# Kernel optimization log

Hardware: AMD Instinct MI355X
Metric: run time of the kernel (lower is better)

Reference implementation:

```python
import jax, jax.numpy as jnp
import numpy as np

N_HEAD = 8
HEAD_DIM = 32  # 256 / 8
MASK_VALUE = -10000.0

def setup_inputs() -> dict:
    key = jax.random.key(0)
    k1, k2, k3 = jax.random.split(key, 3)
    B, S, D = 8, 2048, 256
    x = jax.random.normal(k1, (B, S, D), dtype=jnp.float32)
    # kaiming_normal fan_in-based std ~ sqrt(2/fan_in)
    w_qkv = jax.random.normal(k2, (3 * D, D), dtype=jnp.float32) * np.sqrt(2.0 / D)
    b_qkv = jnp.zeros((3 * D,), dtype=jnp.float32)
    w_out = jax.random.normal(k3, (D, D), dtype=jnp.float32) * np.sqrt(2.0 / D)
    b_out = jnp.zeros((D,), dtype=jnp.float32)
    return {"x": x, "w_qkv": w_qkv, "b_qkv": b_qkv, "w_out": w_out, "b_out": b_out}

def reference(x, w_qkv, b_qkv, w_out, b_out):
    B, S, D = x.shape
    qkv = x @ w_qkv.T + b_qkv                      # [B,S,3D]
    q, k, v = jnp.split(qkv, 3, axis=-1)           # each [B,S,D]
    def split_heads(t):
        return t.reshape(B, S, N_HEAD, HEAD_DIM).transpose(0, 2, 1, 3)  # [B,H,S,hd]
    q, k, v = split_heads(q), split_heads(k), split_heads(v)
    scores = jnp.einsum('bhqd,bhkd->bhqk', q, k) / jnp.sqrt(jnp.float32(HEAD_DIM))
    causal = jnp.tril(jnp.ones((S, S), dtype=bool))
    scores = jnp.where(causal[None, None], scores, jnp.float32(MASK_VALUE))
    attn = jax.nn.softmax(scores, axis=-1)          # dropout p=0 (eval)
    out = jnp.einsum('bhqk,bhkd->bhqd', attn, v)    # [B,H,S,hd]
    out = out.transpose(0, 2, 1, 3).reshape(B, S, D)  # merge heads
    out = out @ w_out.T + b_out
    return (out, attn)
```

## Files before the change

kernel.cpp:

```cpp
#include <hip/hip_runtime.h>
#include <cmath>

#define NB 8
#define NS 2048
#define ND 256
#define NH 8
#define HD 32
#define NM (NB*NS)
#define QS_LOG2 (0.17677669529663689f * 1.4426950408889634f)
#define OUT_ATTN ((size_t)NM * ND)

typedef __attribute__((ext_vector_type(8))) short bf16x8;
typedef __attribute__((ext_vector_type(4))) float f32x4;

__device__ __forceinline__ ushort f2b(float f) {
  union { float f; uint32_t u; } v; v.f = f;
  const uint32_t r = (v.u + 0x7FFFu + ((v.u >> 16) & 1u)) >> 16;
  return (ushort)r;
}
__device__ __forceinline__ float b2f(ushort u) {
  union { uint32_t u; float f; } v; v.u = ((uint32_t)u) << 16;
  return v.f;
}

__global__ __launch_bounds__(256) void prep_kernel(
    const float* __restrict__ x, const float* __restrict__ wq,
    const float* __restrict__ wo,
    ushort* __restrict__ xh, ushort* __restrict__ xl,
    ushort* __restrict__ wqh, ushort* __restrict__ wql,
    ushort* __restrict__ woh) {
  const int g = blockIdx.x * 256 + threadIdx.x;
  if (g < 1048576) {
    const float4 v = ((const float4*)x)[g];
    ushort4 h, l;
    h.x = f2b(v.x); l.x = f2b(v.x - b2f(h.x));
    h.y = f2b(v.y); l.y = f2b(v.y - b2f(h.y));
    h.z = f2b(v.z); l.z = f2b(v.z - b2f(h.z));
    h.w = f2b(v.w); l.w = f2b(v.w - b2f(h.w));
    ((ushort4*)xh)[g] = h; ((ushort4*)xl)[g] = l;
  } else if (g < 1048576 + 49152) {
    const int t = g - 1048576;
    const float4 v = ((const float4*)wq)[t];
    ushort4 h, l;
    h.x = f2b(v.x); l.x = f2b(v.x - b2f(h.x));
    h.y = f2b(v.y); l.y = f2b(v.y - b2f(h.y));
    h.z = f2b(v.z); l.z = f2b(v.z - b2f(h.z));
    h.w = f2b(v.w); l.w = f2b(v.w - b2f(h.w));
    ((ushort4*)wqh)[t] = h; ((ushort4*)wql)[t] = l;
  } else if (g < 1048576 + 49152 + 16384) {
    const int t = g - (1048576 + 49152);
    const float4 v = ((const float4*)wo)[t];
    ushort4 h;
    h.x = f2b(v.x); h.y = f2b(v.y); h.z = f2b(v.z); h.w = f2b(v.w);
    ((ushort4*)woh)[t] = h;
  }
}

__global__ __launch_bounds__(256) void qkv_kernel(
    const ushort* __restrict__ xh, const ushort* __restrict__ xl,
    const ushort* __restrict__ wqh, const ushort* __restrict__ wql,
    const float* __restrict__ bias,
    ushort* __restrict__ Qb, ushort* __restrict__ Kb, ushort* __restrict__ Vt) {
  __shared__ ushort Bh[128][40];
  __shared__ ushort Bl[128][40];
  const int m0 = blockIdx.x * 64;
  const int n0 = blockIdx.y * 128;
  const int tid  = threadIdx.x;
  const int w = tid >> 6, lane = tid & 63;
  const int a = lane & 15, qd = lane >> 4;
  const int srow = tid & 127, sop = tid >> 7;
  const f32x4 zero4 = {0.f, 0.f, 0.f, 0.f};
  f32x4 acc[8] = {zero4, zero4, zero4, zero4, zero4, zero4, zero4, zero4};

  const size_t arow = (size_t)(m0 + w*16 + a) * ND;
  const ushort* __restrict__ bsrc = (sop ? wql : wqh) + (size_t)(n0 + srow) * ND;

  for (int ks = 0; ks < 8; ++ks) {
    const int kofs = ks * 32;
    const bf16x8 t0 = *(const bf16x8*)&bsrc[kofs + 0];
    const bf16x8 t1 = *(const bf16x8*)&bsrc[kofs + 8];
    const bf16x8 t2 = *(const bf16x8*)&bsrc[kofs + 16];
    const bf16x8 t3 = *(const bf16x8*)&bsrc[kofs + 24];
    const bf16x8 ah = *(const bf16x8*)&xh[arow + kofs + qd*8];
    const bf16x8 al = *(const bf16x8*)&xl[arow + kofs + qd*8];
    __syncthreads();
    ushort (* __restrict__ Bs)[40] = sop ? Bl : Bh;
    *(bf16x8*)&Bs[srow][0]  = t0;
    *(bf16x8*)&Bs[srow][8]  = t1;
    *(bf16x8*)&Bs[srow][16] = t2;
    *(bf16x8*)&Bs[srow][24] = t3;
    __syncthreads();
#pragma unroll
    for (int nt = 0; nt < 8; ++nt) {
      const bf16x8 bhf = *(const bf16x8*)&Bh[nt*16 + a][qd*8];
      const bf16x8 blf = *(const bf16x8*)&Bl[nt*16 + a][qd*8];
      acc[nt] = __builtin_amdgcn_mfma_f32_16x16x32_bf16(al, bhf, acc[nt], 0, 0, 0);
      acc[nt] = __builtin_amdgcn_mfma_f32_16x16x32_bf16(ah, blf, acc[nt], 0, 0, 0);
      acc[nt] = __builtin_amdgcn_mfma_f32_16x16x32_bf16(ah, bhf, acc[nt], 0, 0, 0);
    }
  }

  const int mbase = m0 + w*16 + qd*4;
  const int bb = mbase >> 11, ss = mbase & 2047;
#pragma unroll
  for (int nt = 0; nt < 8; ++nt) {
    const int n = n0 + nt*16 + a;
    const int which = n >> 8;
    const int h = (n >> 5) & 7, e0 = n & 31;
    const float bz = bias[n];
    if (which < 2) {
      const float scl = (which == 0) ? QS_LOG2 : 1.0f;
      ushort* const dst = ((which == 0) ? Qb : Kb) + (size_t)(bb*NH + h) * NS * HD;
#pragma unroll
      for (int r = 0; r < 4; ++r)
        dst[(size_t)(ss + r) * HD + e0] = f2b((acc[nt][r] + bz) * scl);
    } else {
      ushort4 o;
      o.x = f2b(acc[nt][0] + bz);
      o.y = f2b(acc[nt][1] + bz);
      o.z = f2b(acc[nt][2] + bz);
      o.w = f2b(acc[nt][3] + bz);
      *(ushort4*)&Vt[((size_t)(bb*NH + h)*HD + e0) * NS + ss] = o;
    }
  }
}

__global__ __launch_bounds__(256) void attn_kernel(
    const ushort* __restrict__ Qb, const ushort* __restrict__ Kb,
    const ushort* __restrict__ Vt, float* __restrict__ attn,
    ushort* __restrict__ Om) {
  __shared__ float Ps[64][68];
  const int bh = blockIdx.x;
  const int by = blockIdx.y;
  const int qt = (by & 1) ? (by >> 1) : (NS/64 - 1 - (by >> 1));
  const int q0 = qt * 64;
  const int lane = threadIdx.x & 63;
  const int w    = threadIdx.x >> 6;
  const int a    = lane & 15;
  const int qd   = lane >> 4;
  const ushort* __restrict__ Qh = Qb + (size_t)bh * NS * HD;
  const ushort* __restrict__ Kh = Kb + (size_t)bh * NS * HD;
  const ushort* __restrict__ Vh = Vt + (size_t)bh * HD * NS;

  const f32x4 zero4 = {0.f, 0.f, 0.f, 0.f};
  const bf16x8 qf = *(const bf16x8*)&Qh[(size_t)(q0 + w*16 + a) * HD + qd*8];
  float* const attnRow = attn + ((size_t)bh * NS + q0) * NS;

  bf16x8 kf[4], kn[4], vf[4], vn[4];
#pragma unroll
  for (int jt = 0; jt < 4; ++jt)
    kf[jt] = *(const bf16x8*)&Kh[(size_t)(jt*16 + a) * HD + qd*8];

  float l_l[4] = {0.f, 0.f, 0.f, 0.f};
  int zt = qt + 1;
  for (int kt = 0; kt <= qt; ++kt) {
    const bool diag = (kt == qt);
    const int lim = diag ? w : 3;
    if (kt < qt) {
      const int k0n = (kt + 1) * 64;
#pragma unroll
      for (int jt = 0; jt < 4; ++jt)
        kn[jt] = *(const bf16x8*)&Kh[(size_t)(k0n + jt*16 + a) * HD + qd*8];
    }
    if (zt < NS / 64) {
      const int z0 = zt * 64;
#pragma unroll
      for (int i = 0; i < 4; ++i)
        __builtin_nontemporal_store(zero4,
            (f32x4*)&attnRow[(size_t)(w*16 + i*4 + qd) * NS + z0 + a*4]);
      ++zt;
    }
#pragma unroll
    for (int jt = 0; jt < 4; ++jt) {
      if (jt > lim) continue;
      const f32x4 s = __builtin_amdgcn_mfma_f32_16x16x32_bf16(qf, kf[jt], zero4, 0, 0, 0);
      if (diag && jt == w) {
#pragma unroll
        for (int r = 0; r < 4; ++r)
          l_l[r] += (a > qd*4 + r) ? 0.f : exp2f(s[r]);
      } else {
#pragma unroll
        for (int r = 0; r < 4; ++r)
          l_l[r] += exp2f(s[r]);
      }
    }
#pragma unroll
    for (int jt = 0; jt < 4; ++jt) kf[jt] = kn[jt];
  }

#pragma unroll
  for (int jt = 0; jt < 4; ++jt)
    kf[jt] = *(const bf16x8*)&Kh[(size_t)(jt*16 + a) * HD + qd*8];
  vf[0] = *(const bf16x8*)&Vh[(size_t)(a)      * NS + qd*8];
  vf[1] = *(const bf16x8*)&Vh[(size_t)(16 + a) * NS + qd*8];
  vf[2] = *(const bf16x8*)&Vh[(size_t)(a)      * NS + 32 + qd*8];
  vf[3] = *(const bf16x8*)&Vh[(size_t)(16 + a) * NS + 32 + qd*8];

  for (; zt < NS / 64; ++zt) {
    const int z0 = zt * 64;
#pragma unroll
    for (int i = 0; i < 4; ++i)
      __builtin_nontemporal_store(zero4,
          (f32x4*)&attnRow[(size_t)(w*16 + i*4 + qd) * NS + z0 + a*4]);
  }

  float mc[4];
#pragma unroll
  for (int r = 0; r < 4; ++r) {
    float c = l_l[r];
#pragma unroll
    for (int off = 1; off < 16; off <<= 1) c += __shfl_xor(c, off);
    mc[r] = log2f(c);
  }

  f32x4 oc0 = zero4, oc1 = zero4;

  for (int kt = 0; kt <= qt; ++kt) {
    const int k0 = kt * 64;
    const bool diag = (kt == qt);
    const int lim = diag ? w : 3;

    if (kt < qt) {
      const int k0n = k0 + 64;
#pragma unroll
      for (int jt = 0; jt < 4; ++jt)
        kn[jt] = *(const bf16x8*)&Kh[(size_t)(k0n + jt*16 + a) * HD + qd*8];
      vn[0] = *(const bf16x8*)&Vh[(size_t)(a)      * NS + k0n + qd*8];
      vn[1] = *(const bf16x8*)&Vh[(size_t)(16 + a) * NS + k0n + qd*8];
      vn[2] = *(const bf16x8*)&Vh[(size_t)(a)      * NS + k0n + 32 + qd*8];
      vn[3] = *(const bf16x8*)&Vh[(size_t)(16 + a) * NS + k0n + 32 + qd*8];
    }

#pragma unroll
    for (int jt = 0; jt < 4; ++jt) {
      if (jt > lim) {
#pragma unroll
        for (int r = 0; r < 4; ++r)
          Ps[w*16 + qd*4 + r][jt*16 + a] = 0.f;
        continue;
      }
      const f32x4 s = __builtin_amdgcn_mfma_f32_16x16x32_bf16(qf, kf[jt], zero4, 0, 0, 0);
      if (diag && jt == w) {
#pragma unroll
        for (int r = 0; r < 4; ++r)
          Ps[w*16 + qd*4 + r][jt*16 + a] =
              (a > qd*4 + r) ? 0.f : exp2f(s[r] - mc[r]);
      } else {
#pragma unroll
        for (int r = 0; r < 4; ++r)
          Ps[w*16 + qd*4 + r][jt*16 + a] = exp2f(s[r] - mc[r]);
      }
    }

#pragma unroll
    for (int i = 0; i < 4; ++i) {
      const int row16 = i*4 + qd;
      const f32x4 pv = *(const f32x4*)&Ps[w*16 + row16][a*4];
      __builtin_nontemporal_store(pv,
          (f32x4*)&attnRow[(size_t)(w*16 + row16) * NS + k0 + a*4]);
    }

#pragma unroll
    for (int half = 0; half < 2; ++half) {
      const float4 p0 = *(const float4*)&Ps[w*16 + a][half*32 + qd*8];
      const float4 p1 = *(const float4*)&Ps[w*16 + a][half*32 + qd*8 + 4];
      bf16x8 pa;
      pa[0] = (short)f2b(p0.x); pa[1] = (short)f2b(p0.y);
      pa[2] = (short)f2b(p0.z); pa[3] = (short)f2b(p0.w);
      pa[4] = (short)f2b(p1.x); pa[5] = (short)f2b(p1.y);
      pa[6] = (short)f2b(p1.z); pa[7] = (short)f2b(p1.w);
      oc0 = __builtin_amdgcn_mfma_f32_16x16x32_bf16(pa, half ? vf[2] : vf[0], oc0, 0, 0, 0);
      oc1 = __builtin_amdgcn_mfma_f32_16x16x32_bf16(pa, half ? vf[3] : vf[1], oc1, 0, 0, 0);
    }
#pragma unroll
    for (int jt = 0; jt < 4; ++jt) { kf[jt] = kn[jt]; vf[jt] = vn[jt]; }
  }

  const int bb = bh >> 3, hh = bh & 7;
#pragma unroll
  for (int r = 0; r < 4; ++r) {
    const size_t om = (size_t)(bb * NS + q0 + w*16 + qd*4 + r) * ND + hh*32;
    Om[om + a]      = f2b(oc0[r]);
    Om[om + 16 + a] = f2b(oc1[r]);
  }
}

__global__ __launch_bounds__(256) void proj_kernel(
    const ushort* __restrict__ Om, const ushort* __restrict__ woh,
    const float* __restrict__ bias, float* __restrict__ out) {
  const int m0 = blockIdx.x * 64;
  const int nb = blockIdx.y * 64;
  const int w = threadIdx.x >> 6, lane = threadIdx.x & 63;
  const int a = lane & 15, qd = lane >> 4;
  const f32x4 zero4 = {0.f, 0.f, 0.f, 0.f};
  f32x4 acc[4] = {zero4, zero4, zero4, zero4};
  const size_t arow = (size_t)(m0 + w*16 + a) * ND;
#pragma unroll
  for (int ks = 0; ks < 8; ++ks) {
    const int kofs = ks * 32 + qd * 8;
    const bf16x8 af = *(const bf16x8*)&Om[arow + kofs];
#pragma unroll
    for (int nt = 0; nt < 4; ++nt) {
      const bf16x8 bfg = *(const bf16x8*)&woh[(size_t)(nb + nt*16 + a) * ND + kofs];
      acc[nt] = __builtin_amdgcn_mfma_f32_16x16x32_bf16(af, bfg, acc[nt], 0, 0, 0);
    }
  }
#pragma unroll
  for (int nt = 0; nt < 4; ++nt) {
    const int n = nb + nt*16 + a;
    const float bz = bias[n];
#pragma unroll
    for (int r = 0; r < 4; ++r)
      out[(size_t)(m0 + w*16 + qd*4 + r) * ND + n] = acc[nt][r] + bz;
  }
}

extern "C" void kernel_launch(void* const* d_in, const int* in_sizes, int n_in,
                              void* d_out, int out_size, void* d_ws, size_t ws_size,
                              hipStream_t stream) {
  const float* x     = (const float*)d_in[0];
  const float* w_qkv = (const float*)d_in[1];
  const float* b_qkv = (const float*)d_in[2];
  const float* w_out = (const float*)d_in[3];
  const float* b_out = (const float*)d_in[4];
  float* out  = (float*)d_out;
  float* attn = out + OUT_ATTN;

  ushort* u = (ushort*)d_ws;
  const size_t SZH = (size_t)NB * NH * NS * HD;
  ushort* Qb  = u;  u += SZH;
  ushort* Kb  = u;  u += SZH;
  ushort* Vt  = u;  u += SZH;
  ushort* Om  = u;  u += SZH;
  ushort* xh  = u;  u += SZH;
  ushort* xl  = u;  u += SZH;
  ushort* wqh = u;  u += (size_t)768 * ND;
  ushort* wql = u;  u += (size_t)768 * ND;
  ushort* woh = u;  u += (size_t)ND * ND;

  prep_kernel<<<4352, 256, 0, stream>>>(x, w_qkv, w_out, xh, xl, wqh, wql, woh);
  qkv_kernel<<<dim3(NM / 64, 768 / 128), 256, 0, stream>>>(xh, xl, wqh, wql, b_qkv, Qb, Kb, Vt);
  attn_kernel<<<dim3(NB * NH, NS / 64), 256, 0, stream>>>(Qb, Kb, Vt, attn, Om);
  proj_kernel<<<dim3(NM / 64, ND / 64), 256, 0, stream>>>(Om, woh, b_out, out);
}
```

Baseline: 311.8 us.

## Fuse x bf16 split into QKV GEMM and widen N tile to 256

Drops the prep pass that split x into hi/lo bf16 arrays in workspace. The QKV kernel now reads fp32 x directly and converts it to hi/lo in registers. The N tile grows from 128 to 256 so each block covers exactly one of Q, K or V, which lets the epilogue branch per block instead of per column. This removes the x conversion pass and its extra global round trip, and halves the number of re-reads of x across N-blocks. In exchange it doubles accumulator registers and shared memory per block, which may lower occupancy.

```diff
diff --git a/kernel.cpp b/kernel.cpp
--- a/kernel.cpp
+++ b/kernel.cpp
@@ -24,31 +24,20 @@
 }
 
 __global__ __launch_bounds__(256) void prep_kernel(
-    const float* __restrict__ x, const float* __restrict__ wq,
-    const float* __restrict__ wo,
-    ushort* __restrict__ xh, ushort* __restrict__ xl,
+    const float* __restrict__ wq, const float* __restrict__ wo,
     ushort* __restrict__ wqh, ushort* __restrict__ wql,
     ushort* __restrict__ woh) {
   const int g = blockIdx.x * 256 + threadIdx.x;
-  if (g < 1048576) {
-    const float4 v = ((const float4*)x)[g];
+  if (g < 49152) {
+    const float4 v = ((const float4*)wq)[g];
     ushort4 h, l;
     h.x = f2b(v.x); l.x = f2b(v.x - b2f(h.x));
     h.y = f2b(v.y); l.y = f2b(v.y - b2f(h.y));
     h.z = f2b(v.z); l.z = f2b(v.z - b2f(h.z));
     h.w = f2b(v.w); l.w = f2b(v.w - b2f(h.w));
-    ((ushort4*)xh)[g] = h; ((ushort4*)xl)[g] = l;
-  } else if (g < 1048576 + 49152) {
-    const int t = g - 1048576;
-    const float4 v = ((const float4*)wq)[t];
-    ushort4 h, l;
-    h.x = f2b(v.x); l.x = f2b(v.x - b2f(h.x));
-    h.y = f2b(v.y); l.y = f2b(v.y - b2f(h.y));
-    h.z = f2b(v.z); l.z = f2b(v.z - b2f(h.z));
-    h.w = f2b(v.w); l.w = f2b(v.w - b2f(h.w));
-    ((ushort4*)wqh)[t] = h; ((ushort4*)wql)[t] = l;
-  } else if (g < 1048576 + 49152 + 16384) {
-    const int t = g - (1048576 + 49152);
+    ((ushort4*)wqh)[g] = h; ((ushort4*)wql)[g] = l;
+  } else if (g < 49152 + 16384) {
+    const int t = g - 49152;
     const float4 v = ((const float4*)wo)[t];
     ushort4 h;
     h.x = f2b(v.x); h.y = f2b(v.y); h.z = f2b(v.z); h.w = f2b(v.w);
@@ -57,41 +46,60 @@
 }
 
 __global__ __launch_bounds__(256) void qkv_kernel(
-    const ushort* __restrict__ xh, const ushort* __restrict__ xl,
+    const float* __restrict__ x,
     const ushort* __restrict__ wqh, const ushort* __restrict__ wql,
     const float* __restrict__ bias,
     ushort* __restrict__ Qb, ushort* __restrict__ Kb, ushort* __restrict__ Vt) {
-  __shared__ ushort Bh[128][40];
-  __shared__ ushort Bl[128][40];
+  __shared__ ushort Bh[256][40];
+  __shared__ ushort Bl[256][40];
   const int m0 = blockIdx.x * 64;
-  const int n0 = blockIdx.y * 128;
+  const int n0 = blockIdx.y * 256;
   const int tid  = threadIdx.x;
   const int w = tid >> 6, lane = tid & 63;
   const int a = lane & 15, qd = lane >> 4;
-  const int srow = tid & 127, sop = tid >> 7;
   const f32x4 zero4 = {0.f, 0.f, 0.f, 0.f};
-  f32x4 acc[8] = {zero4, zero4, zero4, zero4, zero4, zero4, zero4, zero4};
+  f32x4 acc[16];
+#pragma unroll
+  for (int i = 0; i < 16; ++i) acc[i] = zero4;
 
   const size_t arow = (size_t)(m0 + w*16 + a) * ND;
-  const ushort* __restrict__ bsrc = (sop ? wql : wqh) + (size_t)(n0 + srow) * ND;
+  const ushort* __restrict__ bh_src = wqh + (size_t)(n0 + tid) * ND;
+  const ushort* __restrict__ bl_src = wql + (size_t)(n0 + tid) * ND;
 
   for (int ks = 0; ks < 8; ++ks) {
     const int kofs = ks * 32;
-    const bf16x8 t0 = *(const bf16x8*)&bsrc[kofs + 0];
-    const bf16x8 t1 = *(const bf16x8*)&bsrc[kofs + 8];
-    const bf16x8 t2 = *(const bf16x8*)&bsrc[kofs + 16];
-    const bf16x8 t3 = *(const bf16x8*)&bsrc[kofs + 24];
-    const bf16x8 ah = *(const bf16x8*)&xh[arow + kofs + qd*8];
-    const bf16x8 al = *(const bf16x8*)&xl[arow + kofs + qd*8];
+    const bf16x8 h0 = *(const bf16x8*)&bh_src[kofs + 0];
+    const bf16x8 h1 = *(const bf16x8*)&bh_src[kofs + 8];
+    const bf16x8 h2 = *(const bf16x8*)&bh_src[kofs + 16];
+    const bf16x8 h3 = *(const bf16x8*)&bh_src[kofs + 24];
+    const bf16x8 l0 = *(const bf16x8*)&bl_src[kofs + 0];
+    const bf16x8 l1 = *(const bf16x8*)&bl_src[kofs + 8];
+    const bf16x8 l2 = *(const bf16x8*)&bl_src[kofs + 16];
+    const bf16x8 l3 = *(const bf16x8*)&bl_src[kofs + 24];
+    const float4 xa = *(const float4*)&x[arow + kofs + qd*8];
+    const float4 xb = *(const float4*)&x[arow + kofs + qd*8 + 4];
+    bf16x8 ah, al;
+    {
+      const float xv[8] = {xa.x, xa.y, xa.z, xa.w, xb.x, xb.y, xb.z, xb.w};
+#pragma unroll
+      for (int i = 0; i < 8; ++i) {
+        const ushort hi = f2b(xv[i]);
+        ah[i] = (short)hi;
+        al[i] = (short)f2b(xv[i] - b2f(hi));
+      }
+    }
     __syncthreads();
-    ushort (* __restrict__ Bs)[40] = sop ? Bl : Bh;
-    *(bf16x8*)&Bs[srow][0]  = t0;
-    *(bf16x8*)&Bs[srow][8]  = t1;
-    *(bf16x8*)&Bs[srow][16] = t2;
-    *(bf16x8*)&Bs[srow][24] = t3;
+    *(bf16x8*)&Bh[tid][0]  = h0;
+    *(bf16x8*)&Bh[tid][8]  = h1;
+    *(bf16x8*)&Bh[tid][16] = h2;
+    *(bf16x8*)&Bh[tid][24] = h3;
+    *(bf16x8*)&Bl[tid][0]  = l0;
+    *(bf16x8*)&Bl[tid][8]  = l1;
+    *(bf16x8*)&Bl[tid][16] = l2;
+    *(bf16x8*)&Bl[tid][24] = l3;
     __syncthreads();
 #pragma unroll
-    for (int nt = 0; nt < 8; ++nt) {
+    for (int nt = 0; nt < 16; ++nt) {
       const bf16x8 bhf = *(const bf16x8*)&Bh[nt*16 + a][qd*8];
       const bf16x8 blf = *(const bf16x8*)&Bl[nt*16 + a][qd*8];
       acc[nt] = __builtin_amdgcn_mfma_f32_16x16x32_bf16(al, bhf, acc[nt], 0, 0, 0);
@@ -100,21 +108,26 @@
     }
   }
 
+  const int which = blockIdx.y;
   const int mbase = m0 + w*16 + qd*4;
   const int bb = mbase >> 11, ss = mbase & 2047;
-#pragma unroll
-  for (int nt = 0; nt < 8; ++nt) {
-    const int n = n0 + nt*16 + a;
-    const int which = n >> 8;
-    const int h = (n >> 5) & 7, e0 = n & 31;
-    const float bz = bias[n];
-    if (which < 2) {
-      const float scl = (which == 0) ? QS_LOG2 : 1.0f;
-      ushort* const dst = ((which == 0) ? Qb : Kb) + (size_t)(bb*NH + h) * NS * HD;
+  if (which < 2) {
+    const float scl = (which == 0) ? QS_LOG2 : 1.0f;
+    ushort* const base = ((which == 0) ? Qb : Kb) + (size_t)(bb*NH) * NS * HD;
+#pragma unroll
+    for (int nt = 0; nt < 16; ++nt) {
+      const int h = nt >> 1, e0 = (nt & 1)*16 + a;
+      const float bz = bias[n0 + nt*16 + a];
+      ushort* const dst = base + (size_t)h * NS * HD;
 #pragma unroll
       for (int r = 0; r < 4; ++r)
         dst[(size_t)(ss + r) * HD + e0] = f2b((acc[nt][r] + bz) * scl);
-    } else {
+    }
+  } else {
+#pragma unroll
+    for (int nt = 0; nt < 16; ++nt) {
+      const int h = nt >> 1, e0 = (nt & 1)*16 + a;
+      const float bz = bias[n0 + nt*16 + a];
       ushort4 o;
       o.x = f2b(acc[nt][0] + bz);
       o.y = f2b(acc[nt][1] + bz);
@@ -332,14 +345,12 @@
   ushort* Kb  = u;  u += SZH;
   ushort* Vt  = u;  u += SZH;
   ushort* Om  = u;  u += SZH;
-  ushort* xh  = u;  u += SZH;
-  ushort* xl  = u;  u += SZH;
   ushort* wqh = u;  u += (size_t)768 * ND;
   ushort* wql = u;  u += (size_t)768 * ND;
   ushort* woh = u;  u += (size_t)ND * ND;
 
-  prep_kernel<<<4352, 256, 0, stream>>>(x, w_qkv, w_out, xh, xl, wqh, wql, woh);
-  qkv_kernel<<<dim3(NM / 64, 768 / 128), 256, 0, stream>>>(xh, xl, wqh, wql, b_qkv, Qb, Kb, Vt);
+  prep_kernel<<<256, 256, 0, stream>>>(w_qkv, w_out, wqh, wql, woh);
+  qkv_kernel<<<dim3(NM / 64, 3), 256, 0, stream>>>(x, wqh, wql, b_qkv, Qb, Kb, Vt);
   attn_kernel<<<dim3(NB * NH, NS / 64), 256, 0, stream>>>(Qb, Kb, Vt, attn, Om);
   proj_kernel<<<dim3(NM / 64, ND / 64), 256, 0, stream>>>(Om, woh, b_out, out);
 }
```

New measurement: 325.5 us. +4.4%, slower.

## Software-pipeline PV MFMA one tile behind QK and add wave priority hints

Applied to the files above, without the earlier changes.

Double-buffers the shared P tile so each iteration's P@V MFMA runs on the previous tile's probabilities, letting the exp and QK work of tile kt overlap with the PV work of tile kt-1. V is now loaded for the current tile and consumed in the next iteration, with a drain step after the loop. It also wraps the MFMA/exp sections in s_setprio to favour compute waves over store-issuing ones. The cost is twice the LDS for P, which can lower occupancy, plus changed register pressure. The kernel is likely bound by the large attention-matrix write, so any gain may be limited.

```diff
diff --git a/kernel.cpp b/kernel.cpp
--- a/kernel.cpp
+++ b/kernel.cpp
@@ -129,7 +129,7 @@
     const ushort* __restrict__ Qb, const ushort* __restrict__ Kb,
     const ushort* __restrict__ Vt, float* __restrict__ attn,
     ushort* __restrict__ Om) {
-  __shared__ float Ps[64][68];
+  __shared__ float Ps[2][64][68];
   const int bh = blockIdx.x;
   const int by = blockIdx.y;
   const int qt = (by & 1) ? (by >> 1) : (NS/64 - 1 - (by >> 1));
@@ -146,7 +146,7 @@
   const bf16x8 qf = *(const bf16x8*)&Qh[(size_t)(q0 + w*16 + a) * HD + qd*8];
   float* const attnRow = attn + ((size_t)bh * NS + q0) * NS;
 
-  bf16x8 kf[4], kn[4], vf[4], vn[4];
+  bf16x8 kf[4], kn[4], vf[4], vp[4];
 #pragma unroll
   for (int jt = 0; jt < 4; ++jt)
     kf[jt] = *(const bf16x8*)&Kh[(size_t)(jt*16 + a) * HD + qd*8];
@@ -170,6 +170,7 @@
             (f32x4*)&attnRow[(size_t)(w*16 + i*4 + qd) * NS + z0 + a*4]);
       ++zt;
     }
+    __builtin_amdgcn_s_setprio(1);
 #pragma unroll
     for (int jt = 0; jt < 4; ++jt) {
       if (jt > lim) continue;
@@ -184,6 +185,7 @@
           l_l[r] += exp2f(s[r]);
       }
     }
+    __builtin_amdgcn_s_setprio(0);
 #pragma unroll
     for (int jt = 0; jt < 4; ++jt) kf[jt] = kn[jt];
   }
@@ -214,6 +216,7 @@
   }
 
   f32x4 oc0 = zero4, oc1 = zero4;
+  int buf = 0;
 
   for (int kt = 0; kt <= qt; ++kt) {
     const int k0 = kt * 64;
@@ -225,55 +228,82 @@
 #pragma unroll
       for (int jt = 0; jt < 4; ++jt)
         kn[jt] = *(const bf16x8*)&Kh[(size_t)(k0n + jt*16 + a) * HD + qd*8];
-      vn[0] = *(const bf16x8*)&Vh[(size_t)(a)      * NS + k0n + qd*8];
-      vn[1] = *(const bf16x8*)&Vh[(size_t)(16 + a) * NS + k0n + qd*8];
-      vn[2] = *(const bf16x8*)&Vh[(size_t)(a)      * NS + k0n + 32 + qd*8];
-      vn[3] = *(const bf16x8*)&Vh[(size_t)(16 + a) * NS + k0n + 32 + qd*8];
-    }
-
+    }
+    if (kt > 0) {
+      vf[0] = *(const bf16x8*)&Vh[(size_t)(a)      * NS + k0 + qd*8];
+      vf[1] = *(const bf16x8*)&Vh[(size_t)(16 + a) * NS + k0 + qd*8];
+      vf[2] = *(const bf16x8*)&Vh[(size_t)(a)      * NS + k0 + 32 + qd*8];
+      vf[3] = *(const bf16x8*)&Vh[(size_t)(16 + a) * NS + k0 + 32 + qd*8];
+    }
+
+    __builtin_amdgcn_s_setprio(1);
 #pragma unroll
     for (int jt = 0; jt < 4; ++jt) {
       if (jt > lim) {
 #pragma unroll
         for (int r = 0; r < 4; ++r)
-          Ps[w*16 + qd*4 + r][jt*16 + a] = 0.f;
+          Ps[buf][w*16 + qd*4 + r][jt*16 + a] = 0.f;
         continue;
       }
       const f32x4 s = __builtin_amdgcn_mfma_f32_16x16x32_bf16(qf, kf[jt], zero4, 0, 0, 0);
       if (diag && jt == w) {
 #pragma unroll
         for (int r = 0; r < 4; ++r)
-          Ps[w*16 + qd*4 + r][jt*16 + a] =
+          Ps[buf][w*16 + qd*4 + r][jt*16 + a] =
               (a > qd*4 + r) ? 0.f : exp2f(s[r] - mc[r]);
       } else {
 #pragma unroll
         for (int r = 0; r < 4; ++r)
-          Ps[w*16 + qd*4 + r][jt*16 + a] = exp2f(s[r] - mc[r]);
+          Ps[buf][w*16 + qd*4 + r][jt*16 + a] = exp2f(s[r] - mc[r]);
       }
     }
+    __builtin_amdgcn_s_setprio(0);
 
 #pragma unroll
     for (int i = 0; i < 4; ++i) {
       const int row16 = i*4 + qd;
-      const f32x4 pv = *(const f32x4*)&Ps[w*16 + row16][a*4];
+      const f32x4 pv = *(const f32x4*)&Ps[buf][w*16 + row16][a*4];
       __builtin_nontemporal_store(pv,
           (f32x4*)&attnRow[(size_t)(w*16 + row16) * NS + k0 + a*4]);
     }
 
+    if (kt > 0) {
+      __builtin_amdgcn_s_setprio(1);
+#pragma unroll
+      for (int half = 0; half < 2; ++half) {
+        const float4 p0 = *(const float4*)&Ps[buf ^ 1][w*16 + a][half*32 + qd*8];
+        const float4 p1 = *(const float4*)&Ps[buf ^ 1][w*16 + a][half*32 + qd*8 + 4];
+        bf16x8 pa;
+        pa[0] = (short)f2b(p0.x); pa[1] = (short)f2b(p0.y);
+        pa[2] = (short)f2b(p0.z); pa[3] = (short)f2b(p0.w);
+        pa[4] = (short)f2b(p1.x); pa[5] = (short)f2b(p1.y);
+        pa[6] = (short)f2b(p1.z); pa[7] = (short)f2b(p1.w);
+        oc0 = __builtin_amdgcn_mfma_f32_16x16x32_bf16(pa, half ? vp[2] : vp[0], oc0, 0, 0, 0);
+        oc1 = __builtin_amdgcn_mfma_f32_16x16x32_bf16(pa, half ? vp[3] : vp[1], oc1, 0, 0, 0);
+      }
+      __builtin_amdgcn_s_setprio(0);
+    }
+
+#pragma unroll
+    for (int jt = 0; jt < 4; ++jt) { kf[jt] = kn[jt]; vp[jt] = vf[jt]; }
+    buf ^= 1;
+  }
+
+  {
+    __builtin_amdgcn_s_setprio(1);
 #pragma unroll
     for (int half = 0; half < 2; ++half) {
-      const float4 p0 = *(const float4*)&Ps[w*16 + a][half*32 + qd*8];
-      const float4 p1 = *(const float4*)&Ps[w*16 + a][half*32 + qd*8 + 4];
+      const float4 p0 = *(const float4*)&Ps[buf ^ 1][w*16 + a][half*32 + qd*8];
+      const float4 p1 = *(const float4*)&Ps[buf ^ 1][w*16 + a][half*32 + qd*8 + 4];
       bf16x8 pa;
       pa[0] = (short)f2b(p0.x); pa[1] = (short)f2b(p0.y);
       pa[2] = (short)f2b(p0.z); pa[3] = (short)f2b(p0.w);
       pa[4] = (short)f2b(p1.x); pa[5] = (short)f2b(p1.y);
       pa[6] = (short)f2b(p1.z); pa[7] = (short)f2b(p1.w);
-      oc0 = __builtin_amdgcn_mfma_f32_16x16x32_bf16(pa, half ? vf[2] : vf[0], oc0, 0, 0, 0);
-      oc1 = __builtin_amdgcn_mfma_f32_16x16x32_bf16(pa, half ? vf[3] : vf[1], oc1, 0, 0, 0);
-    }
-#pragma unroll
-    for (int jt = 0; jt < 4; ++jt) { kf[jt] = kn[jt]; vf[jt] = vn[jt]; }
+      oc0 = __builtin_amdgcn_mfma_f32_16x16x32_bf16(pa, half ? vp[2] : vp[0], oc0, 0, 0, 0);
+      oc1 = __builtin_amdgcn_mfma_f32_16x16x32_bf16(pa, half ? vp[3] : vp[1], oc1, 0, 0, 0);
+    }
+    __builtin_amdgcn_s_setprio(0);
   }
 
   const int bb = bh >> 3, hh = bh & 7;
```

After: 307.9 us, median of 2. No clear change (-1.2%).
